# Performance work log

Hardware: AMD Instinct MI355X
Metric: run time of the kernel (lower is better)

## Reference

```python
import jax, jax.numpy as jnp
import numpy as np

D_MODEL = 1024
NUM_HEADS = 16
D_K = D_MODEL // NUM_HEADS


def setup_inputs() -> dict:
    key = jax.random.key(0)
    ks = jax.random.split(key, 9)
    s = 1.0 / np.sqrt(D_MODEL)
    x = jax.random.normal(ks[0], (2, 2048, D_MODEL), dtype=jnp.float32)
    Wq = jax.random.uniform(ks[1], (D_MODEL, D_MODEL), jnp.float32, -s, s)
    bq = jax.random.uniform(ks[2], (D_MODEL,), jnp.float32, -s, s)
    Wk = jax.random.uniform(ks[3], (D_MODEL, D_MODEL), jnp.float32, -s, s)
    bk = jax.random.uniform(ks[4], (D_MODEL,), jnp.float32, -s, s)
    Wv = jax.random.uniform(ks[5], (D_MODEL, D_MODEL), jnp.float32, -s, s)
    bv = jax.random.uniform(ks[6], (D_MODEL,), jnp.float32, -s, s)
    Wo = jax.random.uniform(ks[7], (D_MODEL, D_MODEL), jnp.float32, -s, s)
    bo = jax.random.uniform(ks[8], (D_MODEL,), jnp.float32, -s, s)
    return {"x": x, "Wq": Wq, "bq": bq, "Wk": Wk, "bk": bk,
            "Wv": Wv, "bv": bv, "Wo": Wo, "bo": bo}


def reference(x, Wq, bq, Wk, bk, Wv, bv, Wo, bo):
    B, S, _ = x.shape
    # torch Linear: y = x @ W.T + b
    def proj(W, b):
        h = x @ W.T + b                       # [B,S,D]
        return h.reshape(B, S, NUM_HEADS, D_K).transpose(0, 2, 1, 3)  # [B,H,S,Dk]
    Q = proj(Wq, bq)
    K = proj(Wk, bk)
    V = proj(Wv, bv)
    scale = 1.0 / np.sqrt(D_K)
    scores = jnp.einsum('bhqd,bhkd->bhqk', Q, K) * scale   # [B,H,S,S]
    causal = jnp.triu(jnp.ones((S, S), dtype=bool), k=1)   # True above diag
    scores = jnp.where(causal, -jnp.inf, scores)
    probs = jax.nn.softmax(scores, axis=-1)
    out = jnp.einsum('bhqk,bhkd->bhqd', probs, V)          # [B,H,S,Dk]
    out = out.transpose(0, 2, 1, 3).reshape(B, S, NUM_HEADS * D_K)
    return out @ Wo.T + bo
```

## Files before the change

kernel.cpp:

```cpp
#include <hip/hip_runtime.h>

typedef unsigned short u16;
typedef __attribute__((ext_vector_type(8))) short short8;
typedef __attribute__((ext_vector_type(4))) float floatx4;

__device__ __forceinline__ u16 f2bf(float x){
  union { float f; unsigned u; } v; v.f = x;
  unsigned r = v.u + 0x7fffu + ((v.u >> 16) & 1u);
  return (u16)(r >> 16);
}

__device__ __forceinline__ unsigned cvt_pk_bf16(float lo, float hi){
  unsigned r;
  asm("v_cvt_pk_bf16_f32 %0, %1, %2" : "=v"(r) : "v"(lo), "v"(hi));
  return r;
}

__device__ __forceinline__ void gld16(const u16* g, u16* l){
  __builtin_amdgcn_global_load_lds(
      (const __attribute__((address_space(1))) void*)g,
      (__attribute__((address_space(3))) void*)l, 16, 0, 0);
}

__global__ void k_cvt_all(const float* __restrict__ x,
                          const float* __restrict__ wq, const float* __restrict__ wk,
                          const float* __restrict__ wv, const float* __restrict__ wo,
                          u16* __restrict__ xb, u16* __restrict__ wqb, u16* __restrict__ wkb,
                          u16* __restrict__ wvb, u16* __restrict__ wob){
  const int i = blockIdx.x * 256 + threadIdx.x;
  const float* s; u16* d; int off;
  if (i < 1048576) { s = x; d = xb; off = i; }
  else {
    const int j = i - 1048576;
    const int wsel = j >> 18;
    off = j & 262143;
    s = (wsel==0) ? wq : (wsel==1) ? wk : (wsel==2) ? wv : wo;
    d = (wsel==0) ? wqb : (wsel==1) ? wkb : (wsel==2) ? wvb : wob;
  }
  const float4 f = ((const float4*)s)[off];
  unsigned lo = (unsigned)f2bf(f.x) | ((unsigned)f2bf(f.y) << 16);
  unsigned hi = (unsigned)f2bf(f.z) | ((unsigned)f2bf(f.w) << 16);
  ((uint2*)d)[off] = make_uint2(lo, hi);
}

__global__ __launch_bounds__(256) void k_gemm_qkv(
    const u16* __restrict__ A,
    const u16* __restrict__ Wq, const u16* __restrict__ Wk, const u16* __restrict__ Wv,
    const float* __restrict__ bq, const float* __restrict__ bk, const float* __restrict__ bv,
    u16* __restrict__ Qo, u16* __restrict__ Ko, u16* __restrict__ Vo)
{
  const int bid = (int)blockIdx.x;
  const int xcd = bid & 7;
  const int i5  = bid >> 3;
  const int xb_ = ((xcd >> 2) << 2) + (i5 & 3);
  const int rest = i5 >> 2;
  const int yb_ = ((xcd & 3) << 3) + (rest & 7);
  const int mode = rest >> 3;

  const u16* W      = (mode==1) ? Wk : (mode==2) ? Wv : Wq;
  const float* bias = (mode==1) ? bk : (mode==2) ? bv : bq;

  __shared__ u16 lA[2][4096];
  __shared__ u16 lB[2][4096];

  const int tid  = threadIdx.x;
  const int row0 = yb_ * 128;
  const int col0 = xb_ * 128;

  const int srow = tid >> 2;
  const int sgp  = tid & 3;
  const int sgl  = sgp ^ ((srow >> 1) & 3);
  const u16* ga0 = A + (row0 + srow)      * 1024 + sgl * 8;
  const u16* ga1 = A + (row0 + srow + 64) * 1024 + sgl * 8;
  const u16* gb0 = W + (col0 + srow)      * 1024 + sgl * 8;
  const u16* gb1 = W + (col0 + srow + 64) * 1024 + sgl * 8;

  const int l  = tid & 63, w = tid >> 6;
  const int wr = w >> 1,  wc = w & 1;
  const int lr = l & 15,  grp = l >> 4;
  const int sw = (lr >> 1) & 3;
  int aoff[4], boff[4];
#pragma unroll
  for (int m = 0; m < 4; ++m) aoff[m] = (wr*64 + m*16 + lr)*32 + ((grp ^ sw) * 8);
#pragma unroll
  for (int n = 0; n < 4; ++n) boff[n] = (wc*64 + n*16 + lr)*32 + ((grp ^ sw) * 8);

  floatx4 acc[4][4];
#pragma unroll
  for (int m = 0; m < 4; ++m)
#pragma unroll
    for (int n = 0; n < 4; ++n) acc[m][n] = (floatx4){0.f, 0.f, 0.f, 0.f};

#define STAGE(buf, kt_) do { \
    const int k0_ = (kt_) * 32; \
    gld16(ga0 + k0_, &lA[(buf)][tid*8]); \
    gld16(ga1 + k0_, &lA[(buf)][2048 + tid*8]); \
    gld16(gb0 + k0_, &lB[(buf)][tid*8]); \
    gld16(gb1 + k0_, &lB[(buf)][2048 + tid*8]); \
  } while (0)

  STAGE(0, 0);
  __syncthreads();
  for (int kt = 0; kt < 32; ++kt) {
    const int cur = kt & 1;
    if (kt < 31) STAGE(cur ^ 1, kt + 1);
    short8 af[4], bf[4];
#pragma unroll
    for (int m = 0; m < 4; ++m) af[m] = *(const short8*)&lA[cur][aoff[m]];
#pragma unroll
    for (int n = 0; n < 4; ++n) bf[n] = *(const short8*)&lB[cur][boff[n]];
#pragma unroll
    for (int m = 0; m < 4; ++m)
#pragma unroll
      for (int n = 0; n < 4; ++n)
        acc[m][n] = __builtin_amdgcn_mfma_f32_16x16x32_bf16(af[m], bf[n], acc[m][n], 0, 0, 0);
    __syncthreads();
  }
#undef STAGE

  const float sc = (mode == 0) ? 0.18033688011112042f : 1.0f;
  u16* dst = (mode == 0) ? Qo : (mode == 1) ? Ko : Vo;
#pragma unroll
  for (int n = 0; n < 4; ++n) {
    const int cg = col0 + wc*64 + n*16 + lr;
    const float bb = bias[cg];
    const int h = cg >> 6, d = cg & 63;
#pragma unroll
    for (int m = 0; m < 4; ++m) {
#pragma unroll
      for (int j = 0; j < 4; ++j) {
        const int rg = row0 + wr*64 + m*16 + grp*4 + j;
        const int b = rg >> 11, s5 = rg & 2047;
        const float val = (acc[m][n][j] + bb) * sc;
        int idx;
        if (mode == 2) idx = ((b*16 + h)*64 + d)*2048 + s5;
        else           idx = ((b*16 + h)*2048 + s5)*64 + d;
        dst[idx] = f2bf(val);
      }
    }
  }
}

__global__ __launch_bounds__(256) void k_gemm_o(
    const u16* __restrict__ A, const u16* __restrict__ W,
    const float* __restrict__ bias, float* __restrict__ Fo)
{
  const int bid = (int)blockIdx.x;
  const int xcd = bid & 7;
  const int i5  = bid >> 3;
  const int xb_ = ((xcd >> 2) << 2) + (i5 & 3);
  const int yb_ = ((xcd & 3) << 4) + (i5 >> 2);

  __shared__ u16 lA[2][2048];
  __shared__ u16 lB[2][4096];

  const int tid  = threadIdx.x;
  const int row0 = yb_ * 64;
  const int col0 = xb_ * 128;

  const int srow = tid >> 2;
  const int sgp  = tid & 3;
  const int sgl  = sgp ^ ((srow >> 1) & 3);
  const u16* ga0 = A + (row0 + srow)      * 1024 + sgl * 8;
  const u16* gb0 = W + (col0 + srow)      * 1024 + sgl * 8;
  const u16* gb1 = W + (col0 + srow + 64) * 1024 + sgl * 8;

  const int l  = tid & 63, w = tid >> 6;
  const int wr = w >> 1,  wc = w & 1;
  const int lr = l & 15,  grp = l >> 4;
  const int sw = (lr >> 1) & 3;
  int aoff[2], boff[4];
#pragma unroll
  for (int m = 0; m < 2; ++m) aoff[m] = (wr*32 + m*16 + lr)*32 + ((grp ^ sw) * 8);
#pragma unroll
  for (int n = 0; n < 4; ++n) boff[n] = (wc*64 + n*16 + lr)*32 + ((grp ^ sw) * 8);

  floatx4 acc[2][4];
#pragma unroll
  for (int m = 0; m < 2; ++m)
#pragma unroll
    for (int n = 0; n < 4; ++n) acc[m][n] = (floatx4){0.f, 0.f, 0.f, 0.f};

#define STAGE(buf, kt_) do { \
    const int k0_ = (kt_) * 32; \
    gld16(ga0 + k0_, &lA[(buf)][tid*8]); \
    gld16(gb0 + k0_, &lB[(buf)][tid*8]); \
    gld16(gb1 + k0_, &lB[(buf)][2048 + tid*8]); \
  } while (0)

  STAGE(0, 0);
  __syncthreads();
  for (int kt = 0; kt < 32; ++kt) {
    const int cur = kt & 1;
    if (kt < 31) STAGE(cur ^ 1, kt + 1);
    short8 af[2], bf[4];
#pragma unroll
    for (int m = 0; m < 2; ++m) af[m] = *(const short8*)&lA[cur][aoff[m]];
#pragma unroll
    for (int n = 0; n < 4; ++n) bf[n] = *(const short8*)&lB[cur][boff[n]];
#pragma unroll
    for (int m = 0; m < 2; ++m)
#pragma unroll
      for (int n = 0; n < 4; ++n)
        acc[m][n] = __builtin_amdgcn_mfma_f32_16x16x32_bf16(af[m], bf[n], acc[m][n], 0, 0, 0);
    __syncthreads();
  }
#undef STAGE

#pragma unroll
  for (int n = 0; n < 4; ++n) {
    const int cg = col0 + wc*64 + n*16 + lr;
    const float bb = bias[cg];
#pragma unroll
    for (int m = 0; m < 2; ++m) {
      const int rg = row0 + wr*32 + m*16 + grp*4;
#pragma unroll
      for (int j = 0; j < 4; ++j)
        Fo[(rg + j) * 1024 + cg] = acc[m][n][j] + bb;
    }
  }
}

__global__ __launch_bounds__(256, 4) void k_attn(
    const u16* __restrict__ Q, const u16* __restrict__ K,
    const u16* __restrict__ V, u16* __restrict__ O)
{
  __shared__ u16 lK[2][4096];
  __shared__ u16 lV[2][4096];
  __shared__ u16 lP[4][1024];

  const int tid = threadIdx.x;
  const int bid = (int)blockIdx.x;
  const int xcd = bid & 7, r = bid >> 3;
  const int bh = xcd * 4 + (r >> 4);
  const int pr = r & 15;

  const int l = tid & 63, w = tid >> 6;
  const int lr = l & 15, grp = l >> 4;

  const u16* Qh = Q + (size_t)bh * 2048 * 64;
  const u16* Kh = K + (size_t)bh * 2048 * 64;
  const u16* Vh = V + (size_t)bh * 64 * 2048;

  const int srow = tid >> 3, sgp = tid & 7;
  const int sgl = sgp ^ (srow & 7);
  u16* lPw = &lP[w][0];
  const int swz = lr & 7;
  const int b = bh >> 4, h = bh & 15;

#define STAGEKV(buf, kt_) do { \
    gld16(Kh + ((kt_)*64 + srow     )*64 + sgl*8, &lK[(buf)][tid*8]); \
    gld16(Kh + ((kt_)*64 + srow + 32)*64 + sgl*8, &lK[(buf)][2048 + tid*8]); \
    gld16(Vh + (srow     )*2048 + (kt_)*64 + sgl*8, &lV[(buf)][tid*8]); \
    gld16(Vh + (srow + 32)*2048 + (kt_)*64 + sgl*8, &lV[(buf)][2048 + tid*8]); \
  } while (0)

#pragma unroll
  for (int pass = 0; pass < 2; ++pass) {
    const int qt = pass ? pr : (31 - pr);
    const int qw0 = qt * 64 + w * 16;
    const int nkt = qt + 1;

    short8 qf[2];
#pragma unroll
    for (int kk = 0; kk < 2; ++kk)
      qf[kk] = *(const short8*)(Qh + (qw0 + lr)*64 + kk*32 + grp*8);

    floatx4 accO[4];
    float mrow = -1e30f, lrow = 0.f;
#pragma unroll
    for (int dn = 0; dn < 4; ++dn) accO[dn] = (floatx4){0.f, 0.f, 0.f, 0.f};

    STAGEKV(0, 0);
    __syncthreads();

    for (int kt = 0; kt < nkt; ++kt) {
      const int cur = kt & 1;
      if (kt + 1 < nkt) STAGEKV(cur ^ 1, kt + 1);
      const int kb = kt * 64;

      floatx4 st[4];
#pragma unroll
      for (int n = 0; n < 4; ++n) st[n] = (floatx4){0.f, 0.f, 0.f, 0.f};
#pragma unroll
      for (int n = 0; n < 4; ++n) {
        const int key = n*16 + lr;
#pragma unroll
        for (int kk = 0; kk < 2; ++kk) {
          const int gp = (kk*4 + grp) ^ (key & 7);
          short8 kf = *(const short8*)&lK[cur][key*64 + gp*8];
          st[n] = __builtin_amdgcn_mfma_f32_16x16x32_bf16(kf, qf[kk], st[n], 0, 0, 0);
        }
      }

      const int lim = qw0 + lr - kb;
      if (63 > lim) {
#pragma unroll
        for (int n = 0; n < 4; ++n)
#pragma unroll
          for (int j = 0; j < 4; ++j)
            if (n*16 + grp*4 + j > lim) st[n][j] = -1e30f;
      }

      float mt = st[0][0];
#pragma unroll
      for (int n = 0; n < 4; ++n)
#pragma unroll
        for (int j = 0; j < 4; ++j) mt = fmaxf(mt, st[n][j]);
      mt = fmaxf(mt, __shfl_xor(mt, 16));
      mt = fmaxf(mt, __shfl_xor(mt, 32));
      const float mn = fmaxf(mrow, mt);
      const float alpha = exp2f(mrow - mn);
      mrow = mn;
      float ps = 0.f;
#pragma unroll
      for (int n = 0; n < 4; ++n)
#pragma unroll
        for (int j = 0; j < 4; ++j) {
          const float p = exp2f(st[n][j] - mn);
          st[n][j] = p;
          ps += p;
        }
      ps += __shfl_xor(ps, 16);
      ps += __shfl_xor(ps, 32);
      lrow = lrow * alpha + ps;
#pragma unroll
      for (int dn = 0; dn < 4; ++dn) accO[dn] *= alpha;

#pragma unroll
      for (int n = 0; n < 4; ++n)
#pragma unroll
        for (int p2 = 0; p2 < 2; ++p2) {
          const unsigned pk = cvt_pk_bf16(st[n][2*p2], st[n][2*p2+1]);
          const int pg = (2*n + (grp >> 1)) ^ swz;
          ((unsigned*)lPw)[lr*32 + pg*4 + (grp & 1)*2 + p2] = pk;
        }

      asm volatile("s_waitcnt lgkmcnt(0)" ::: "memory");

      short8 pa[2];
#pragma unroll
      for (int kk = 0; kk < 2; ++kk)
        pa[kk] = *(const short8*)&lPw[lr*64 + (((kk*4 + grp) ^ swz) * 8)];

#pragma unroll
      for (int dn = 0; dn < 4; ++dn) {
        const int d = dn*16 + lr;
#pragma unroll
        for (int kk = 0; kk < 2; ++kk) {
          const int gp = (kk*4 + grp) ^ (d & 7);
          short8 vf = *(const short8*)&lV[cur][d*64 + gp*8];
          accO[dn] = __builtin_amdgcn_mfma_f32_16x16x32_bf16(vf, pa[kk], accO[dn], 0, 0, 0);
        }
      }
      __syncthreads();
    }

    const float inv = 1.0f / lrow;
    const int token = b*2048 + qw0 + lr;
#pragma unroll
    for (int dn = 0; dn < 4; ++dn)
#pragma unroll
      for (int p2 = 0; p2 < 2; ++p2) {
        const unsigned pk = cvt_pk_bf16(accO[dn][2*p2] * inv, accO[dn][2*p2+1] * inv);
        *(unsigned*)&O[token*1024 + h*64 + dn*16 + grp*4 + 2*p2] = pk;
      }
  }
#undef STAGEKV
}

extern "C" void kernel_launch(void* const* d_in, const int* in_sizes, int n_in,
                              void* d_out, int out_size, void* d_ws, size_t ws_size,
                              hipStream_t stream) {
  const float* x  = (const float*)d_in[0];
  const float* Wq = (const float*)d_in[1];
  const float* bq = (const float*)d_in[2];
  const float* Wk = (const float*)d_in[3];
  const float* bk = (const float*)d_in[4];
  const float* Wv = (const float*)d_in[5];
  const float* bv = (const float*)d_in[6];
  const float* Wo = (const float*)d_in[7];
  const float* bo = (const float*)d_in[8];
  float* out = (float*)d_out;

  char* ws = (char*)d_ws;
  u16* xb  = (u16*)(ws + 0);
  u16* wqb = (u16*)(ws + 8388608);
  u16* wkb = (u16*)(ws + 10485760);
  u16* wvb = (u16*)(ws + 12582912);
  u16* wob = (u16*)(ws + 14680064);
  u16* Qb  = (u16*)(ws + 16777216);
  u16* Kb  = (u16*)(ws + 25165824);
  u16* Vb  = (u16*)(ws + 33554432);
  u16* Ab  = (u16*)(ws + 41943040);

  k_cvt_all<<<dim3(8192), 256, 0, stream>>>(x, Wq, Wk, Wv, Wo, xb, wqb, wkb, wvb, wob);

  k_gemm_qkv<<<dim3(768), 256, 0, stream>>>(xb, wqb, wkb, wvb, bq, bk, bv, Qb, Kb, Vb);

  k_attn<<<dim3(512), 256, 0, stream>>>(Qb, Kb, Vb, Ab);

  k_gemm_o<<<dim3(512), 256, 0, stream>>>(Ab, wob, bo, out);
}
```

Measured before the change: 126.0 us.

## Process two KV tiles per barrier with 4-deep LDS ring and lazy rescale

Expands the K/V LDS buffers from double to quad buffering and processes two key tiles per loop iteration, halving the number of block-wide barriers and prefetching two tiles ahead. The online softmax now skips the cross-lane max reduction and accumulator rescale when no lane's tile max exceeds the running max, and defers the row-sum shuffle reduction to the end. The larger shared memory footprint lowers the occupancy hint from 4 to 2 blocks per CU, trading latency hiding via occupancy for deeper prefetch and fewer syncs.

```diff
diff --git a/kernel.cpp b/kernel.cpp
--- a/kernel.cpp
+++ b/kernel.cpp
@@ -221,12 +221,12 @@
   }
 }
 
-__global__ __launch_bounds__(256, 4) void k_attn(
+__global__ __launch_bounds__(256, 2) void k_attn(
     const u16* __restrict__ Q, const u16* __restrict__ K,
     const u16* __restrict__ V, u16* __restrict__ O)
 {
-  __shared__ u16 lK[2][4096];
-  __shared__ u16 lV[2][4096];
+  __shared__ u16 lK[4][4096];
+  __shared__ u16 lV[4][4096];
   __shared__ u16 lP[4][1024];
 
   const int tid = threadIdx.x;
@@ -272,91 +272,102 @@
     for (int dn = 0; dn < 4; ++dn) accO[dn] = (floatx4){0.f, 0.f, 0.f, 0.f};
 
     STAGEKV(0, 0);
+    if (nkt > 1) STAGEKV(1, 1);
     __syncthreads();
 
-    for (int kt = 0; kt < nkt; ++kt) {
-      const int cur = kt & 1;
-      if (kt + 1 < nkt) STAGEKV(cur ^ 1, kt + 1);
-      const int kb = kt * 64;
-
-      floatx4 st[4];
-#pragma unroll
-      for (int n = 0; n < 4; ++n) st[n] = (floatx4){0.f, 0.f, 0.f, 0.f};
-#pragma unroll
-      for (int n = 0; n < 4; ++n) {
-        const int key = n*16 + lr;
-#pragma unroll
-        for (int kk = 0; kk < 2; ++kk) {
-          const int gp = (kk*4 + grp) ^ (key & 7);
-          short8 kf = *(const short8*)&lK[cur][key*64 + gp*8];
-          st[n] = __builtin_amdgcn_mfma_f32_16x16x32_bf16(kf, qf[kk], st[n], 0, 0, 0);
+    for (int kt2 = 0; kt2 < nkt; kt2 += 2) {
+      if (kt2 + 2 < nkt) STAGEKV((kt2 + 2) & 3, kt2 + 2);
+      if (kt2 + 3 < nkt) STAGEKV((kt2 + 3) & 3, kt2 + 3);
+
+#pragma unroll
+      for (int half = 0; half < 2; ++half) {
+        const int kt = kt2 + half;
+        if (half == 1 && kt >= nkt) break;
+        const int cur = kt & 3;
+        const int kb = kt * 64;
+
+        floatx4 st[4];
+#pragma unroll
+        for (int n = 0; n < 4; ++n) st[n] = (floatx4){0.f, 0.f, 0.f, 0.f};
+#pragma unroll
+        for (int n = 0; n < 4; ++n) {
+          const int key = n*16 + lr;
+#pragma unroll
+          for (int kk = 0; kk < 2; ++kk) {
+            const int gp = (kk*4 + grp) ^ (key & 7);
+            short8 kf = *(const short8*)&lK[cur][key*64 + gp*8];
+            st[n] = __builtin_amdgcn_mfma_f32_16x16x32_bf16(kf, qf[kk], st[n], 0, 0, 0);
+          }
         }
-      }
-
-      const int lim = qw0 + lr - kb;
-      if (63 > lim) {
+
+        const int lim = qw0 + lr - kb;
+        if (63 > lim) {
+#pragma unroll
+          for (int n = 0; n < 4; ++n)
+#pragma unroll
+            for (int j = 0; j < 4; ++j)
+              if (n*16 + grp*4 + j > lim) st[n][j] = -1e30f;
+        }
+
+        float mt = st[0][0];
 #pragma unroll
         for (int n = 0; n < 4; ++n)
 #pragma unroll
-          for (int j = 0; j < 4; ++j)
-            if (n*16 + grp*4 + j > lim) st[n][j] = -1e30f;
-      }
-
-      float mt = st[0][0];
-#pragma unroll
-      for (int n = 0; n < 4; ++n)
-#pragma unroll
-        for (int j = 0; j < 4; ++j) mt = fmaxf(mt, st[n][j]);
-      mt = fmaxf(mt, __shfl_xor(mt, 16));
-      mt = fmaxf(mt, __shfl_xor(mt, 32));
-      const float mn = fmaxf(mrow, mt);
-      const float alpha = exp2f(mrow - mn);
-      mrow = mn;
-      float ps = 0.f;
-#pragma unroll
-      for (int n = 0; n < 4; ++n)
-#pragma unroll
-        for (int j = 0; j < 4; ++j) {
-          const float p = exp2f(st[n][j] - mn);
-          st[n][j] = p;
-          ps += p;
+          for (int j = 0; j < 4; ++j) mt = fmaxf(mt, st[n][j]);
+        if (!__all(mt <= mrow)) {
+          float mg = fmaxf(mt, __shfl_xor(mt, 16));
+          mg = fmaxf(mg, __shfl_xor(mg, 32));
+          const float mn = fmaxf(mrow, mg);
+          const float alpha = exp2f(mrow - mn);
+          mrow = mn;
+          lrow *= alpha;
+#pragma unroll
+          for (int dn = 0; dn < 4; ++dn) accO[dn] *= alpha;
         }
-      ps += __shfl_xor(ps, 16);
-      ps += __shfl_xor(ps, 32);
-      lrow = lrow * alpha + ps;
-#pragma unroll
-      for (int dn = 0; dn < 4; ++dn) accO[dn] *= alpha;
-
-#pragma unroll
-      for (int n = 0; n < 4; ++n)
-#pragma unroll
-        for (int p2 = 0; p2 < 2; ++p2) {
-          const unsigned pk = cvt_pk_bf16(st[n][2*p2], st[n][2*p2+1]);
-          const int pg = (2*n + (grp >> 1)) ^ swz;
-          ((unsigned*)lPw)[lr*32 + pg*4 + (grp & 1)*2 + p2] = pk;
-        }
-
-      asm volatile("s_waitcnt lgkmcnt(0)" ::: "memory");
-
-      short8 pa[2];
-#pragma unroll
-      for (int kk = 0; kk < 2; ++kk)
-        pa[kk] = *(const short8*)&lPw[lr*64 + (((kk*4 + grp) ^ swz) * 8)];
-
-#pragma unroll
-      for (int dn = 0; dn < 4; ++dn) {
-        const int d = dn*16 + lr;
-#pragma unroll
-        for (int kk = 0; kk < 2; ++kk) {
-          const int gp = (kk*4 + grp) ^ (d & 7);
-          short8 vf = *(const short8*)&lV[cur][d*64 + gp*8];
-          accO[dn] = __builtin_amdgcn_mfma_f32_16x16x32_bf16(vf, pa[kk], accO[dn], 0, 0, 0);
+        float ps = 0.f;
+#pragma unroll
+        for (int n = 0; n < 4; ++n)
+#pragma unroll
+          for (int j = 0; j < 4; ++j) {
+            const float p = exp2f(st[n][j] - mrow);
+            st[n][j] = p;
+            ps += p;
+          }
+        lrow += ps;
+
+#pragma unroll
+        for (int n = 0; n < 4; ++n)
+#pragma unroll
+          for (int p2 = 0; p2 < 2; ++p2) {
+            const unsigned pk = cvt_pk_bf16(st[n][2*p2], st[n][2*p2+1]);
+            const int pg = (2*n + (grp >> 1)) ^ swz;
+            ((unsigned*)lPw)[lr*32 + pg*4 + (grp & 1)*2 + p2] = pk;
+          }
+
+        asm volatile("s_waitcnt lgkmcnt(0)" ::: "memory");
+
+        short8 pa[2];
+#pragma unroll
+        for (int kk = 0; kk < 2; ++kk)
+          pa[kk] = *(const short8*)&lPw[lr*64 + (((kk*4 + grp) ^ swz) * 8)];
+
+#pragma unroll
+        for (int dn = 0; dn < 4; ++dn) {
+          const int d = dn*16 + lr;
+#pragma unroll
+          for (int kk = 0; kk < 2; ++kk) {
+            const int gp = (kk*4 + grp) ^ (d & 7);
+            short8 vf = *(const short8*)&lV[cur][d*64 + gp*8];
+            accO[dn] = __builtin_amdgcn_mfma_f32_16x16x32_bf16(vf, pa[kk], accO[dn], 0, 0, 0);
+          }
         }
       }
       __syncthreads();
     }
 
-    const float inv = 1.0f / lrow;
+    float lt = lrow + __shfl_xor(lrow, 16);
+    lt += __shfl_xor(lt, 32);
+    const float inv = 1.0f / lt;
     const int token = b*2048 + qw0 + lr;
 #pragma unroll
     for (int dn = 0; dn < 4; ++dn)
```

After: 123.3 us. -2.1%, faster.
